# Optimization experiments

Measured on AMD Instinct MI355X. Metric: run time of the kernel, lower is better.

Reference implementation:

```python
import jax, jax.numpy as jnp
import numpy as np

B, D_IN, D_OUT, HID = 65536, 512, 512, 1024
LEVELS = (1, 4, 16)
BASE_LR = 0.1
LN_EPS = 1e-5


def setup_inputs() -> dict:
    key = jax.random.key(0)
    ks = jax.random.split(key, 20)
    s_in = 1.0 / np.sqrt(D_IN)
    s_h = 1.0 / np.sqrt(HID)
    inp = {
        'x': jax.random.normal(ks[0], (B, D_IN), dtype=jnp.float32),
        'global_step': 16,
        # CMS: 3 residual MLPs (d_in -> hid -> d_in)
        'cms_w1': jax.random.normal(ks[1], (3, HID, D_IN), dtype=jnp.float32) * s_in,
        'cms_b1': jnp.zeros((3, HID), dtype=jnp.float32),
        'cms_w2': jax.random.normal(ks[2], (3, D_IN, HID), dtype=jnp.float32) * s_h,
        'cms_b2': jnp.zeros((3, D_IN), dtype=jnp.float32),
        # gate generator
        'g_metab_w': jax.random.normal(ks[3], (HID, D_IN), dtype=jnp.float32) * s_in,
        'g_metab_b': jnp.zeros((HID,), dtype=jnp.float32),
        'g_sens_w': jax.random.normal(ks[4], (HID, D_IN), dtype=jnp.float32) * s_in,
        'g_sens_b': jnp.zeros((HID,), dtype=jnp.float32),
        'g_gate_w': jax.random.normal(ks[5], (HID, D_IN), dtype=jnp.float32) * s_in,
        'g_gate_b': jnp.zeros((HID,), dtype=jnp.float32),
        'g_out_w': jax.random.normal(ks[6], (3, HID), dtype=jnp.float32) * s_h,
        'g_out_b': jnp.zeros((3,), dtype=jnp.float32),
        # slow / fast weights, layernorm
        'W_slow': jax.random.normal(ks[7], (D_OUT, D_IN), dtype=jnp.float32) * (1.4 * s_in),
        'W_fast': jax.random.normal(ks[8], (D_OUT, D_IN), dtype=jnp.float32) * 0.01,
        'ln_gamma': jnp.ones((D_OUT,), dtype=jnp.float32),
        'ln_beta': jnp.zeros((D_OUT,), dtype=jnp.float32),
    }
    return inp


def reference(x, global_step, cms_w1, cms_b1, cms_w2, cms_b2,
              g_metab_w, g_metab_b, g_sens_w, g_sens_b, g_gate_w, g_gate_b,
              g_out_w, g_out_b, W_slow, W_fast, ln_gamma, ln_beta):
    # --- ContinuumMemorySystem: frequency-gated residual MLPs ---
    out = x
    for i, freq in enumerate(LEVELS):
        if global_step % freq == 0:
            h = jax.nn.relu(jnp.einsum('bd,hd->bh', out, cms_w1[i]) + cms_b1[i])
            out = jnp.einsum('bh,dh->bd', h, cms_w2[i]) + cms_b2[i] + out
    x_cms = out  # [B, D_IN]

    # --- SelfModifyingGates ---
    metab_h = jax.nn.sigmoid(jnp.einsum('bd,hd->bh', x_cms, g_metab_w) + g_metab_b)
    sens_h = jax.nn.sigmoid(jnp.einsum('bd,hd->bh', x_cms, g_sens_w) + g_sens_b)
    gate_h = jax.nn.sigmoid(jnp.einsum('bd,hd->bh', x_cms, g_gate_w) + g_gate_b)
    gates = jax.nn.sigmoid(jnp.einsum('bh,oh->bo', metab_h + sens_h + gate_h, g_out_w) + g_out_b)  # [B,3]
    metab, sens, gate = gates[:, 0], gates[:, 1], gates[:, 2]

    # --- slow / fast paths ---
    slow = jnp.einsum('bd,od->bo', x_cms, W_slow)   # [B, D_OUT]
    fast = jnp.einsum('bd,od->bo', x_cms, W_fast)   # [B, D_OUT]

    # --- Hebbian fast-weight update (no_grad in original) ---
    hebb = jnp.einsum('bo,bd->od', fast, x_cms) / x_cms.shape[0]     # [D_OUT, D_IN]
    forget = jnp.mean(fast ** 2, axis=0)[:, None] * W_fast           # [D_OUT, D_IN]
    rate = jnp.mean(metab) * BASE_LR
    new_W_fast = W_fast + jnp.tanh(hebb - forget) * rate

    # --- combine, per-sample-beta swish, layernorm ---
    combined = slow + fast * gate[:, None]
    beta = 0.5 + sens[:, None] * 2.0
    act = combined * jax.nn.sigmoid(beta * combined)
    mu = jnp.mean(act, axis=-1, keepdims=True)
    var = jnp.mean((act - mu) ** 2, axis=-1, keepdims=True)
    ln_out = (act - mu) * jax.lax.rsqrt(var + LN_EPS) * ln_gamma + ln_beta

    stats = jnp.stack([jnp.mean(metab), jnp.mean(sens), jnp.mean(gate)])
    return ln_out, new_W_fast, stats
```

## Files before the change

### kernel.cpp

```cpp
#include <hip/hip_runtime.h>
#include <hip/hip_bf16.h>
#include <cstdint>
#include <cstddef>

#define NB 65536
#define DD 512
#define HH 1024

typedef __attribute__((ext_vector_type(8))) short short8;
typedef __attribute__((ext_vector_type(4))) short short4v;
typedef __attribute__((ext_vector_type(4))) float f32x4;

__device__ __forceinline__ float bf2f(short s){
  union { float f; unsigned u; } v; v.u = ((unsigned)(unsigned short)s) << 16; return v.f;
}
__device__ __forceinline__ short f2bf(float f){
  union { float f; unsigned u; } v; v.f = f;
  unsigned u = v.u;
  u += 0x7FFFu + ((u >> 16) & 1u);
  return (short)(u >> 16);
}
__device__ __forceinline__ float sigm(float x){ return 1.0f / (1.0f + __expf(-x)); }

__device__ __forceinline__ float rowsum16(float v){
  int x;
  x = __builtin_amdgcn_update_dpp(0, __float_as_int(v), 0x128, 0xF, 0xF, true); v += __int_as_float(x);
  x = __builtin_amdgcn_update_dpp(0, __float_as_int(v), 0x124, 0xF, 0xF, true); v += __int_as_float(x);
  x = __builtin_amdgcn_update_dpp(0, __float_as_int(v), 0x122, 0xF, 0xF, true); v += __int_as_float(x);
  x = __builtin_amdgcn_update_dpp(0, __float_as_int(v), 0x121, 0xF, 0xF, true); v += __int_as_float(x);
  return v;
}

__device__ __forceinline__ int2 xcd_remap(int NX, int G){
  int flat = blockIdx.y*NX + blockIdx.x;
  int l = (flat & 7)*(G>>3) + (flat>>3);
  return make_int2(l / NX, l % NX);
}

#define GLL(srcp, dstp) \
  __builtin_amdgcn_global_load_lds((const __attribute__((address_space(1))) void*)(srcp), \
                                   (__attribute__((address_space(3))) void*)(dstp), 16, 0, 0)

__device__ __forceinline__ void stage128x32s(const short* __restrict__ g, int row0, int ldk, int k0,
                                             short* lds_base, int wave, int lane){
  const int pl = lane>>3, Gp = lane&7;
  const int Gl = Gp ^ pl;
  const int rconst = pl + ((Gl>>2)<<6);
  const int kg = (Gl&3)*8;
#pragma unroll
  for (int i = 0; i < 2; ++i){
    int c = wave*2 + i;
    const short* src = g + (size_t)(row0 + c*8 + rconst)*(size_t)ldk + (size_t)(k0 + kg);
    GLL(src, lds_base + c*512);
  }
}

template<int KTOT>
__device__ __forceinline__ void gemm128(const short* __restrict__ A, const short* __restrict__ W,
        int m0, int n0, short* smem, f32x4 acc[4][4], int wave, int lane)
{
  const int lr = lane & 15, lq = lane>>4;
  const int hiA = wave>>1, hiB = wave&1;
  int aOff[4], bOff[4];
#pragma unroll
  for (int i=0;i<4;++i){
    int pa = i*16 + lr;
    aOff[i] =        pa*64 + (((hiA*4+lq) ^ (pa&7))<<3);
    bOff[i] = 4096 + pa*64 + (((hiB*4+lq) ^ (pa&7))<<3);
  }
  stage128x32s(A, m0, KTOT, 0, smem,        wave, lane);
  stage128x32s(W, n0, KTOT, 0, smem + 4096, wave, lane);
  asm volatile("s_waitcnt vmcnt(0)" ::: "memory");
  __builtin_amdgcn_s_barrier();
  int cur = 0;
#pragma unroll
  for (int k0 = 0; k0 < KTOT; k0 += 32){
    short* buf  = smem + cur*8192;
    short* nbuf = smem + (cur^1)*8192;
    if (k0 + 32 < KTOT){
      stage128x32s(A, m0, KTOT, k0+32, nbuf,        wave, lane);
      stage128x32s(W, n0, KTOT, k0+32, nbuf + 4096, wave, lane);
    }
    short8 af[4], bf[4];
#pragma unroll
    for (int i=0;i<4;++i) af[i] = *(const short8*)&buf[aOff[i]];
#pragma unroll
    for (int i=0;i<4;++i) bf[i] = *(const short8*)&buf[bOff[i]];
    __builtin_amdgcn_s_setprio(1);
#pragma unroll
    for (int mi=0;mi<4;++mi)
#pragma unroll
      for (int ni=0;ni<4;++ni)
        acc[mi][ni] = __builtin_amdgcn_mfma_f32_16x16x32_bf16(af[mi], bf[ni], acc[mi][ni], 0, 0, 0);
    __builtin_amdgcn_s_setprio(0);
    asm volatile("s_waitcnt vmcnt(0)" ::: "memory");
    __builtin_amdgcn_s_barrier();
    cur ^= 1;
  }
}

#define ZERO_ACC(acc) \
  _Pragma("unroll") for (int zi=0;zi<4;++zi) _Pragma("unroll") for (int zj=0;zj<4;++zj) \
    acc[zi][zj] = (f32x4){0.f,0.f,0.f,0.f};

__global__ __launch_bounds__(256, 4) void k_gemm_h(const int* __restrict__ gs, int freq,
     const short* __restrict__ A, const short* __restrict__ W1, const float* __restrict__ b1,
     short* __restrict__ Hout)
{
  if (gs[0] % freq) return;
  __shared__ __align__(16) short smem[16384];
  const int tid = threadIdx.x, wave = tid>>6, lane = tid&63;
  int2 r = xcd_remap(8, 4096);
  const int m0 = r.x*128, n0 = r.y*128;
  f32x4 acc[4][4]; ZERO_ACC(acc);
  gemm128<DD>(A, W1, m0, n0, smem, acc, wave, lane);
  const int wm=(wave>>1)*64, wn=(wave&1)*64;
  const int rbase = m0 + wm + ((lane>>4)<<2);
  const int cbase = n0 + wn + (lane&15);
#pragma unroll
  for (int ni=0;ni<4;++ni){
    const float bias = b1[cbase + ni*16];
#pragma unroll
    for (int mi=0;mi<4;++mi)
#pragma unroll
      for (int rr=0;rr<4;++rr){
        float v = acc[mi][ni][rr] + bias;
        v = v > 0.f ? v : 0.f;
        Hout[(size_t)(rbase + mi*16 + rr)*HH + (cbase + ni*16)] = f2bf(v);
      }
  }
}

__global__ __launch_bounds__(256, 4) void k_gemm_res(const int* __restrict__ gs, int freq,
     const short* __restrict__ Hb, const short* __restrict__ W2, const float* __restrict__ b2,
     short* __restrict__ outb)
{
  if (gs[0] % freq) return;
  __shared__ __align__(16) short smem[16384];
  const int tid = threadIdx.x, wave = tid>>6, lane = tid&63;
  int2 r = xcd_remap(4, 2048);
  const int m0 = r.x*128, n0 = r.y*128;
  f32x4 acc[4][4]; ZERO_ACC(acc);
  gemm128<HH>(Hb, W2, m0, n0, smem, acc, wave, lane);
  const int wm=(wave>>1)*64, wn=(wave&1)*64;
  const int rbase = m0 + wm + ((lane>>4)<<2);
  const int cbase = n0 + wn + (lane&15);
#pragma unroll
  for (int ni=0;ni<4;++ni){
    const float bias = b2[cbase + ni*16];
#pragma unroll
    for (int mi=0;mi<4;++mi)
#pragma unroll
      for (int rr=0;rr<4;++rr){
        size_t off = (size_t)(rbase + mi*16 + rr)*DD + (cbase + ni*16);
        float v = acc[mi][ni][rr] + bias + bf2f(outb[off]);
        outb[off] = f2bf(v);
      }
  }
}

__global__ __launch_bounds__(256, 4) void k_gates(const short* __restrict__ A, const short* __restrict__ WG,
     const float* __restrict__ bm, const float* __restrict__ bs, const float* __restrict__ bg,
     const float* __restrict__ gow, float* __restrict__ pacc)
{
  __shared__ __align__(16) short smem[16384];
  __shared__ float sred[2][128][3];
  const int tid = threadIdx.x, wave = tid>>6, lane = tid&63;
  const int wmh = wave>>1, wnh = wave&1, lr = lane&15, lq = lane>>4;
  int2 r = xcd_remap(24, 12288);
  const int m0 = r.x*128, xj = r.y;
  const int j = xj >> 3, nb = xj & 7;
  const int n0 = nb*128;
  f32x4 acc[4][4]; ZERO_ACC(acc);
  gemm128<DD>(A, WG + (size_t)j*HH*DD, m0, n0, smem, acc, wave, lane);
  const int cb = n0 + wnh*64 + lr;
  const float* bj = (j==0) ? bm : ((j==1) ? bs : bg);
  float gw0[4], gw1[4], gw2[4], bias[4];
#pragma unroll
  for (int nf=0;nf<4;++nf){
    gw0[nf]  = gow[cb + nf*16];
    gw1[nf]  = gow[1024 + cb + nf*16];
    gw2[nf]  = gow[2048 + cb + nf*16];
    bias[nf] = bj[cb + nf*16];
  }
#pragma unroll
  for (int mf=0;mf<4;++mf)
#pragma unroll
    for (int rr=0;rr<4;++rr){
      float s0=0.f, s1=0.f, s2=0.f;
#pragma unroll
      for (int nf=0;nf<4;++nf){
        float v = sigm(acc[mf][nf][rr] + bias[nf]);
        s0 += v*gw0[nf]; s1 += v*gw1[nf]; s2 += v*gw2[nf];
      }
      s0 = rowsum16(s0); s1 = rowsum16(s1); s2 = rowsum16(s2);
      if (lr == 0){
        int lrow = wmh*64 + mf*16 + lq*4 + rr;
        sred[wnh][lrow][0] = s0;
        sred[wnh][lrow][1] = s1;
        sred[wnh][lrow][2] = s2;
      }
    }
  __syncthreads();
  if (tid < 128){
    float* dst = &pacc[((size_t)xj*NB + m0 + tid)*3];
    dst[0] = sred[0][tid][0] + sred[1][tid][0];
    dst[1] = sred[0][tid][1] + sred[1][tid][1];
    dst[2] = sred[0][tid][2] + sred[1][tid][2];
  }
}

__global__ __launch_bounds__(256, 4) void k_slowfast(const short* __restrict__ A,
     const short* __restrict__ WSF,
     short* __restrict__ SB, short* __restrict__ FB, float* __restrict__ f2sum)
{
  __shared__ __align__(16) short smem[16384];
  __shared__ float f2red[128];
  const int tid = threadIdx.x, wave = tid>>6, lane = tid&63;
  int2 r = xcd_remap(8, 4096);
  const int m0 = r.x*128, n0 = r.y*128;
  const bool isfast = (n0 >= 512);
  if (isfast){
    if (tid < 128) f2red[tid] = 0.f;
  }
  f32x4 acc[4][4]; ZERO_ACC(acc);
  gemm128<DD>(A, WSF, m0, n0, smem, acc, wave, lane);
  const int wm=(wave>>1)*64, wn=(wave&1)*64;
  const int rbase = m0 + wm + ((lane>>4)<<2);
  const int ccol0 = wn + (lane&15);
  if (!isfast){
#pragma unroll
    for (int ni=0;ni<4;++ni)
#pragma unroll
      for (int mi=0;mi<4;++mi)
#pragma unroll
        for (int rr=0;rr<4;++rr)
          SB[(size_t)(rbase + mi*16 + rr)*DD + (n0 + ccol0 + ni*16)] = f2bf(acc[mi][ni][rr]);
  } else {
#pragma unroll
    for (int ni=0;ni<4;++ni){
      float p = 0.f;
      const int fcol = n0 + ccol0 + ni*16 - 512;
#pragma unroll
      for (int mi=0;mi<4;++mi)
#pragma unroll
        for (int rr=0;rr<4;++rr){
          float fv = acc[mi][ni][rr];
          FB[(size_t)(rbase + mi*16 + rr)*DD + fcol] = f2bf(fv);
          p += fv*fv;
        }
      atomicAdd(&f2red[ccol0 + ni*16], p);
    }
    __syncthreads();
    if (tid < 128) atomicAdd(&f2sum[(n0-512) + tid], f2red[tid]);
  }
}

__global__ __launch_bounds__(256) void k_hebb(const short* __restrict__ FB,
     const short* __restrict__ XB, float* __restrict__ hebb)
{
  __shared__ __align__(16) short sT[10240];
  const int tid = threadIdx.x, wave = tid>>6, lane = tid&63;
  const int o0 = blockIdx.x*128, d0 = blockIdx.y*128;
  const int bz = blockIdx.z;
  const int tr = tid>>3;
  const int tc = (tid&7)*16;
  const int wm=(wave>>1)*64, wn=(wave&1)*64;
  const int lr = lane & 15, lk = (lane>>4)*8;
  f32x4 acc[4][4];
#pragma unroll
  for (int zi=0;zi<4;++zi)
#pragma unroll
    for (int zj=0;zj<4;++zj) acc[zi][zj] = (f32x4){0.f,0.f,0.f,0.f};
  for (int bb=0; bb<2048; bb+=32){
    const int b0 = bz*2048 + bb;
    __syncthreads();
#pragma unroll
    for (int h=0; h<2; ++h){
      short8 v = *(const short8*)&FB[(size_t)(b0+tr)*DD + o0 + tc + h*8];
#pragma unroll
      for (int j=0;j<8;++j) sT[(tc+h*8+j)*40 + tr] = v[j];
      short8 u = *(const short8*)&XB[(size_t)(b0+tr)*DD + d0 + tc + h*8];
#pragma unroll
      for (int j=0;j<8;++j) sT[5120 + (tc+h*8+j)*40 + tr] = u[j];
    }
    __syncthreads();
    short8 af[4], bf[4];
#pragma unroll
    for (int i=0;i<4;++i) af[i] = *(const short8*)&sT[(wm + i*16 + lr)*40 + lk];
#pragma unroll
    for (int i=0;i<4;++i) bf[i] = *(const short8*)&sT[5120 + (wn + i*16 + lr)*40 + lk];
#pragma unroll
    for (int mi=0;mi<4;++mi)
#pragma unroll
      for (int ni=0;ni<4;++ni)
        acc[mi][ni] = __builtin_amdgcn_mfma_f32_16x16x32_bf16(af[mi], bf[ni], acc[mi][ni], 0,0,0);
  }
  const int rbase = o0 + wm + ((lane>>4)<<2);
  const int cbase = d0 + wn + (lane&15);
#pragma unroll
  for (int mi=0;mi<4;++mi)
#pragma unroll
    for (int ni=0;ni<4;++ni)
#pragma unroll
      for (int r=0;r<4;++r)
        atomicAdd(&hebb[(size_t)(rbase + mi*16 + r)*DD + (cbase + ni*16)], acc[mi][ni][r]);
}

__global__ __launch_bounds__(256) void k_gatefin(const float* __restrict__ pacc,
     const float* __restrict__ gob,
     float* __restrict__ sensb, float* __restrict__ gateb, float* __restrict__ sacc)
{
  __shared__ float red[3][256];
  const int tid = threadIdx.x;
  const int row = blockIdx.x*256 + tid;
  float a0=0.f, a1=0.f, a2=0.f;
#pragma unroll
  for (int sidx=0; sidx<24; ++sidx){
    const float* p = &pacc[((size_t)sidx*NB + row)*3];
    a0 += p[0]; a1 += p[1]; a2 += p[2];
  }
  float m = sigm(a0 + gob[0]);
  float s = sigm(a1 + gob[1]);
  float g = sigm(a2 + gob[2]);
  sensb[row] = s; gateb[row] = g;
  red[0][tid]=m; red[1][tid]=s; red[2][tid]=g;
  __syncthreads();
  for (int off=128; off; off>>=1){
    if (tid < off){
      red[0][tid]+=red[0][tid+off];
      red[1][tid]+=red[1][tid+off];
      red[2][tid]+=red[2][tid+off];
    }
    __syncthreads();
  }
  if (tid < 3) atomicAdd(&sacc[tid], red[tid][0]);
}

__global__ __launch_bounds__(256) void k_epilogue(const short* __restrict__ SB, const short* __restrict__ FB,
     const float* __restrict__ gate, const float* __restrict__ sens,
     const float* __restrict__ gam, const float* __restrict__ bet, float* __restrict__ out,
     const float* __restrict__ hebb, const float* __restrict__ f2sum, const float* __restrict__ sacc,
     const float* __restrict__ Wf, float* __restrict__ outw, float* __restrict__ outstats)
{
  const int tid = threadIdx.x;
  if (blockIdx.x >= 16384){
    const int idx = (blockIdx.x - 16384)*256 + tid;
    const float inv = 1.f/65536.f;
    const float rate = sacc[0] * inv * 0.1f;
    const int o = idx >> 9;
    float w = Wf[idx];
    float h = hebb[idx] * inv;
    float forget = f2sum[o] * inv * w;
    outw[idx] = w + tanhf(h - forget) * rate;
    if (idx < 3) outstats[idx] = sacc[idx] * inv;
    return;
  }
  const int wave = tid>>6, lane = tid&63;
  const int row = blockIdx.x*4 + wave;
  const float g = gate[row], s = sens[row];
  const float bcoef = 0.5f + 2.0f*s;
  const int c0 = lane*8;
  short8 sv = *(const short8*)&SB[(size_t)row*DD + c0];
  short8 fv = *(const short8*)&FB[(size_t)row*DD + c0];
  float a[8]; float sum = 0.f;
#pragma unroll
  for (int j=0;j<8;++j){
    float c = bf2f(sv[j]) + bf2f(fv[j])*g;
    float av = c * sigm(bcoef*c);
    a[j] = av; sum += av;
  }
  for (int off=32; off; off>>=1) sum += __shfl_down(sum, off);
  sum = __shfl(sum, 0);
  const float mu = sum * (1.f/512.f);
  float vs = 0.f;
#pragma unroll
  for (int j=0;j<8;++j){ float d=a[j]-mu; vs += d*d; }
  for (int off=32; off; off>>=1) vs += __shfl_down(vs, off);
  vs = __shfl(vs, 0);
  const float rstd = rsqrtf(vs*(1.f/512.f) + 1e-5f);
  f32x4 o0, o1;
#pragma unroll
  for (int j=0;j<4;++j) o0[j] = (a[j]-mu)*rstd*gam[c0+j] + bet[c0+j];
#pragma unroll
  for (int j=0;j<4;++j) o1[j] = (a[4+j]-mu)*rstd*gam[c0+4+j] + bet[c0+4+j];
  *(f32x4*)&out[(size_t)row*DD + c0]     = o0;
  *(f32x4*)&out[(size_t)row*DD + c0 + 4] = o1;
}

__global__ __launch_bounds__(256) void k_castall(
     const float* __restrict__ w1, const float* __restrict__ w2,
     const float* __restrict__ gmw, const float* __restrict__ gsw, const float* __restrict__ ggw,
     const float* __restrict__ wslow, const float* __restrict__ wfast,
     short* __restrict__ wcW1, short* __restrict__ wcW2, short* __restrict__ wcG,
     short* __restrict__ wcWSF,
     const float* __restrict__ x, short* __restrict__ outb)
{
  const int b = blockIdx.x, t = threadIdx.x;
  if (b >= 20480){
    const int i = (b - 20480)*256 + t;
    f32x4 v = *(const f32x4*)&x[(size_t)i*4];
    short4v bb;
#pragma unroll
    for (int j=0;j<4;++j) bb[j] = f2bf(v[j]);
    *(short4v*)&outb[(size_t)i*4] = bb;
    return;
  }
  const float* src; short* dst; int off;
  if      (b < 6144)  { src=w1;    dst=wcW1;           off=b; }
  else if (b < 12288) { src=w2;    dst=wcW2;           off=b-6144; }
  else if (b < 14336) { src=gmw;   dst=wcG;            off=b-12288; }
  else if (b < 16384) { src=gsw;   dst=wcG+524288;     off=b-14336; }
  else if (b < 18432) { src=ggw;   dst=wcG+1048576;    off=b-16384; }
  else if (b < 19456) { src=wslow; dst=wcWSF;          off=b-18432; }
  else                { src=wfast; dst=wcWSF+262144;   off=b-19456; }
  const int i = off*256 + t;
  dst[i] = f2bf(src[i]);
}

extern "C" void kernel_launch(void* const* d_in, const int* in_sizes, int n_in,
                              void* d_out, int out_size, void* d_ws, size_t ws_size,
                              hipStream_t stream)
{
  const float* x    = (const float*)d_in[0];
  const int*   gs   = (const int*)d_in[1];
  const float* w1   = (const float*)d_in[2];
  const float* b1   = (const float*)d_in[3];
  const float* w2   = (const float*)d_in[4];
  const float* b2   = (const float*)d_in[5];
  const float* gmw  = (const float*)d_in[6];
  const float* gmb  = (const float*)d_in[7];
  const float* gsw  = (const float*)d_in[8];
  const float* gsb  = (const float*)d_in[9];
  const float* ggw  = (const float*)d_in[10];
  const float* ggb  = (const float*)d_in[11];
  const float* gow  = (const float*)d_in[12];
  const float* gob  = (const float*)d_in[13];
  const float* wslow= (const float*)d_in[14];
  const float* wfast= (const float*)d_in[15];
  const float* gam  = (const float*)d_in[16];
  const float* bet  = (const float*)d_in[17];

  char* ws = (char*)d_ws;
  short* outb  = (short*)(ws + 134217728);
  short* hbuf  = (short*)(ws + 201326592);
  short* wcW1  = (short*)(ws + 335544320);
  short* wcW2  = (short*)(ws + 338690048);
  short* wcG   = (short*)(ws + 341835776);
  short* wcWSF = (short*)(ws + 344981504);
  float* hebb  = (float*)(ws + 346030080);
  float* f2sum = (float*)(ws + 347078656);
  float* sacc  = (float*)(ws + 347080704);
  float* sensb = (float*)(ws + 347080960);
  float* gateb = (float*)(ws + 347343104);
  float* pacc  = (float*)(ws + 201326592);
  short* slowb = (short*)(ws + 0);
  short* fastb = (short*)(ws + 67108864);

  float* o_ln = (float*)d_out;
  float* o_wf = o_ln + (size_t)NB*DD;
  float* o_st = o_wf + 262144;

  hipMemsetAsync(hebb, 0, 1048576, stream);
  hipMemsetAsync(f2sum, 0, 2048, stream);
  hipMemsetAsync(sacc, 0, 256, stream);

  k_castall<<<dim3(53248),256,0,stream>>>(w1, w2, gmw, gsw, ggw, wslow, wfast,
                                          wcW1, wcW2, wcG, wcWSF, x, outb);

  const int freqs[3] = {1,4,16};
  for (int lv=0; lv<3; ++lv){
    k_gemm_h  <<<dim3(8,512),256,0,stream>>>(gs, freqs[lv], outb, wcW1 + (size_t)lv*524288, b1 + lv*HH, hbuf);
    k_gemm_res<<<dim3(4,512),256,0,stream>>>(gs, freqs[lv], hbuf, wcW2 + (size_t)lv*524288, b2 + lv*DD, outb);
  }

  k_gates   <<<dim3(24,512),256,0,stream>>>(outb, wcG, gmb, gsb, ggb, gow, pacc);
  k_gatefin <<<dim3(256),256,0,stream>>>(pacc, gob, sensb, gateb, sacc);
  k_slowfast<<<dim3(8,512),256,0,stream>>>(outb, wcWSF, slowb, fastb, f2sum);
  k_hebb    <<<dim3(4,4,32),256,0,stream>>>(fastb, outb, hebb);
  k_epilogue<<<dim3(17408),256,0,stream>>>(slowb, fastb, gateb, sensb, gam, bet, o_ln,
                                           hebb, f2sum, sacc, wfast, o_wf, o_st);
}
```

Before: 1.288 ms.

## Quantize gate GEMM inputs to int8 and use i8 MFMA

Adds per-row int8 quantization kernels for the CMS output and the three gate weight matrices, then rewrites the gate GEMM to use mfma_i32_16x16x64_i8 with double-buffered LDS staging and dequantization in the epilogue. The aim is to halve operand bytes and use the higher int8 MFMA throughput for the largest GEMM. This adds an extra quantization pass over the activations and loses precision in the gate values, which feed the outputs.

```diff
diff --git a/kernel.cpp b/kernel.cpp
--- a/kernel.cpp
+++ b/kernel.cpp
@@ -10,6 +10,7 @@
 typedef __attribute__((ext_vector_type(8))) short short8;
 typedef __attribute__((ext_vector_type(4))) short short4v;
 typedef __attribute__((ext_vector_type(4))) float f32x4;
+typedef __attribute__((ext_vector_type(4))) int int4v;
 
 __device__ __forceinline__ float bf2f(short s){
   union { float f; unsigned u; } v; v.u = ((unsigned)(unsigned short)s) << 16; return v.f;
@@ -52,6 +53,20 @@
     int c = wave*2 + i;
     const short* src = g + (size_t)(row0 + c*8 + rconst)*(size_t)ldk + (size_t)(k0 + kg);
     GLL(src, lds_base + c*512);
+  }
+}
+
+__device__ __forceinline__ void stage128x64q(const char* __restrict__ g, int k0B,
+                                             char* lds_base, int wave, int lane){
+  const int pl = lane>>3, Gp = lane&7;
+  const int Gl = Gp ^ pl;
+  const int rconst = pl + ((Gl>>2)<<6);
+  const int kg = (Gl&3)*16;
+#pragma unroll
+  for (int i = 0; i < 2; ++i){
+    int c = wave*2 + i;
+    const char* src = g + (size_t)(c*8 + rconst)*512 + (size_t)(k0B + kg);
+    GLL(src, lds_base + c*1024);
   }
 }
 
@@ -159,38 +174,136 @@
   }
 }
 
-__global__ __launch_bounds__(256, 4) void k_gates(const short* __restrict__ A, const short* __restrict__ WG,
+__global__ __launch_bounds__(256) void k_quantx(const short* __restrict__ outb,
+     char* __restrict__ x8, float* __restrict__ sxr)
+{
+  const int tid = threadIdx.x, wave = tid>>6, lane = tid&63;
+  const int row = blockIdx.x*4 + wave;
+  short8 v = *(const short8*)&outb[(size_t)row*DD + lane*8];
+  float f[8]; float m = 0.f;
+#pragma unroll
+  for (int j=0;j<8;++j){ f[j] = bf2f(v[j]); m = fmaxf(m, fabsf(f[j])); }
+#pragma unroll
+  for (int off=32; off; off>>=1) m = fmaxf(m, __shfl_xor(m, off));
+  m = fmaxf(m, 1e-20f);
+  const float inv = 127.0f / m;
+  unsigned lo=0, hi=0;
+#pragma unroll
+  for (int j=0;j<4;++j){ int q=(int)rintf(f[j]*inv); q=q>127?127:(q<-127?-127:q); lo |= ((unsigned)(q&255))<<(8*j); }
+#pragma unroll
+  for (int j=0;j<4;++j){ int q=(int)rintf(f[4+j]*inv); q=q>127?127:(q<-127?-127:q); hi |= ((unsigned)(q&255))<<(8*j); }
+  int2 w; w.x=(int)lo; w.y=(int)hi;
+  *(int2*)&x8[(size_t)row*DD + lane*8] = w;
+  if (lane==0) sxr[row] = m * (1.0f/127.0f);
+}
+
+__global__ __launch_bounds__(256) void k_quantw(const float* __restrict__ gmw,
+     const float* __restrict__ gsw, const float* __restrict__ ggw,
+     char* __restrict__ W8, float* __restrict__ swr)
+{
+  const int tid = threadIdx.x, wave = tid>>6, lane = tid&63;
+  const int row = blockIdx.x*4 + wave;
+  const int j = row >> 10;
+  const float* src = (j==0?gmw:(j==1?gsw:ggw)) + (size_t)(row&1023)*DD + lane*8;
+  f32x4 a = *(const f32x4*)&src[0];
+  f32x4 b = *(const f32x4*)&src[4];
+  float f[8] = {a[0],a[1],a[2],a[3],b[0],b[1],b[2],b[3]};
+  float m = 0.f;
+#pragma unroll
+  for (int k=0;k<8;++k) m = fmaxf(m, fabsf(f[k]));
+#pragma unroll
+  for (int off=32; off; off>>=1) m = fmaxf(m, __shfl_xor(m, off));
+  m = fmaxf(m, 1e-20f);
+  const float inv = 127.0f / m;
+  unsigned lo=0, hi=0;
+#pragma unroll
+  for (int k=0;k<4;++k){ int q=(int)rintf(f[k]*inv); q=q>127?127:(q<-127?-127:q); lo |= ((unsigned)(q&255))<<(8*k); }
+#pragma unroll
+  for (int k=0;k<4;++k){ int q=(int)rintf(f[4+k]*inv); q=q>127?127:(q<-127?-127:q); hi |= ((unsigned)(q&255))<<(8*k); }
+  int2 w; w.x=(int)lo; w.y=(int)hi;
+  *(int2*)&W8[(size_t)row*DD + lane*8] = w;
+  if (lane==0) swr[row] = m * (1.0f/127.0f);
+}
+
+__global__ __launch_bounds__(256, 4) void k_gates(const char* __restrict__ X8, const char* __restrict__ W8,
+     const float* __restrict__ sxr, const float* __restrict__ swr,
      const float* __restrict__ bm, const float* __restrict__ bs, const float* __restrict__ bg,
      const float* __restrict__ gow, float* __restrict__ pacc)
 {
-  __shared__ __align__(16) short smem[16384];
+  __shared__ __align__(16) char smemc[32768];
   __shared__ float sred[2][128][3];
   const int tid = threadIdx.x, wave = tid>>6, lane = tid&63;
   const int wmh = wave>>1, wnh = wave&1, lr = lane&15, lq = lane>>4;
   int2 r = xcd_remap(24, 12288);
   const int m0 = r.x*128, xj = r.y;
-  const int j = xj >> 3, nb = xj & 7;
-  const int n0 = nb*128;
-  f32x4 acc[4][4]; ZERO_ACC(acc);
-  gemm128<DD>(A, WG + (size_t)j*HH*DD, m0, n0, smem, acc, wave, lane);
+  const int j = xj >> 3;
+  const int n0 = (xj & 7)*128;
+  int aOff[4], bOff[4];
+#pragma unroll
+  for (int i=0;i<4;++i){
+    int pa = i*16 + lr;
+    aOff[i] =        pa*128 + (((wmh*4+lq) ^ (pa&7))<<4);
+    bOff[i] = 8192 + pa*128 + (((wnh*4+lq) ^ (pa&7))<<4);
+  }
+  const char* aS = X8 + (size_t)m0*DD;
+  const char* bS = W8 + (size_t)xj*128*DD;
+  int4v acc[4][4];
+#pragma unroll
+  for (int zi=0;zi<4;++zi)
+#pragma unroll
+    for (int zj=0;zj<4;++zj) acc[zi][zj] = (int4v){0,0,0,0};
+
+  stage128x64q(aS, 0, smemc,        wave, lane);
+  stage128x64q(bS, 0, smemc + 8192, wave, lane);
+  asm volatile("s_waitcnt vmcnt(0)" ::: "memory");
+  __builtin_amdgcn_s_barrier();
+  int cur = 0;
+#pragma unroll
+  for (int kt = 0; kt < 8; ++kt){
+    char* buf  = smemc + cur*16384;
+    char* nbuf = smemc + (cur^1)*16384;
+    if (kt + 1 < 8){
+      stage128x64q(aS, (kt+1)*64, nbuf,        wave, lane);
+      stage128x64q(bS, (kt+1)*64, nbuf + 8192, wave, lane);
+    }
+    int4v af[4], bf[4];
+#pragma unroll
+    for (int i=0;i<4;++i) af[i] = *(const int4v*)&buf[aOff[i]];
+#pragma unroll
+    for (int i=0;i<4;++i) bf[i] = *(const int4v*)&buf[bOff[i]];
+    __builtin_amdgcn_s_setprio(1);
+#pragma unroll
+    for (int mi=0;mi<4;++mi)
+#pragma unroll
+      for (int ni=0;ni<4;++ni)
+        acc[mi][ni] = __builtin_amdgcn_mfma_i32_16x16x64_i8(af[mi], bf[ni], acc[mi][ni], 0, 0, 0);
+    __builtin_amdgcn_s_setprio(0);
+    asm volatile("s_waitcnt vmcnt(0)" ::: "memory");
+    __builtin_amdgcn_s_barrier();
+    cur ^= 1;
+  }
+
   const int cb = n0 + wnh*64 + lr;
+  const int rbase = m0 + wmh*64 + lq*4;
   const float* bj = (j==0) ? bm : ((j==1) ? bs : bg);
-  float gw0[4], gw1[4], gw2[4], bias[4];
+  float gw0[4], gw1[4], gw2[4], bias[4], sw[4];
 #pragma unroll
   for (int nf=0;nf<4;++nf){
     gw0[nf]  = gow[cb + nf*16];
     gw1[nf]  = gow[1024 + cb + nf*16];
     gw2[nf]  = gow[2048 + cb + nf*16];
     bias[nf] = bj[cb + nf*16];
+    sw[nf]   = swr[(size_t)xj*128 + wnh*64 + lr + nf*16];
   }
 #pragma unroll
   for (int mf=0;mf<4;++mf)
 #pragma unroll
     for (int rr=0;rr<4;++rr){
+      const float sx = sxr[rbase + mf*16 + rr];
       float s0=0.f, s1=0.f, s2=0.f;
 #pragma unroll
       for (int nf=0;nf<4;++nf){
-        float v = sigm(acc[mf][nf][rr] + bias[nf]);
+        float v = sigm((float)acc[mf][nf][rr] * (sx * sw[nf]) + bias[nf]);
         s0 += v*gw0[nf]; s1 += v*gw1[nf]; s2 += v*gw2[nf];
       }
       s0 = rowsum16(s0); s1 = rowsum16(s1); s2 = rowsum16(s2);
@@ -390,15 +503,13 @@
 
 __global__ __launch_bounds__(256) void k_castall(
      const float* __restrict__ w1, const float* __restrict__ w2,
-     const float* __restrict__ gmw, const float* __restrict__ gsw, const float* __restrict__ ggw,
      const float* __restrict__ wslow, const float* __restrict__ wfast,
-     short* __restrict__ wcW1, short* __restrict__ wcW2, short* __restrict__ wcG,
-     short* __restrict__ wcWSF,
+     short* __restrict__ wcW1, short* __restrict__ wcW2, short* __restrict__ wcWSF,
      const float* __restrict__ x, short* __restrict__ outb)
 {
   const int b = blockIdx.x, t = threadIdx.x;
-  if (b >= 20480){
-    const int i = (b - 20480)*256 + t;
+  if (b >= 14336){
+    const int i = (b - 14336)*256 + t;
     f32x4 v = *(const f32x4*)&x[(size_t)i*4];
     short4v bb;
 #pragma unroll
@@ -409,11 +520,8 @@
   const float* src; short* dst; int off;
   if      (b < 6144)  { src=w1;    dst=wcW1;           off=b; }
   else if (b < 12288) { src=w2;    dst=wcW2;           off=b-6144; }
-  else if (b < 14336) { src=gmw;   dst=wcG;            off=b-12288; }
-  else if (b < 16384) { src=gsw;   dst=wcG+524288;     off=b-14336; }
-  else if (b < 18432) { src=ggw;   dst=wcG+1048576;    off=b-16384; }
-  else if (b < 19456) { src=wslow; dst=wcWSF;          off=b-18432; }
-  else                { src=wfast; dst=wcWSF+262144;   off=b-19456; }
+  else if (b < 13312) { src=wslow; dst=wcWSF;          off=b-12288; }
+  else                { src=wfast; dst=wcWSF+262144;   off=b-13312; }
   const int i = off*256 + t;
   dst[i] = f2bf(src[i]);
 }
@@ -442,17 +550,20 @@
   const float* bet  = (const float*)d_in[17];
 
   char* ws = (char*)d_ws;
+  char*  x8    = (char*)(ws + 0);
   short* outb  = (short*)(ws + 134217728);
   short* hbuf  = (short*)(ws + 201326592);
   short* wcW1  = (short*)(ws + 335544320);
   short* wcW2  = (short*)(ws + 338690048);
-  short* wcG   = (short*)(ws + 341835776);
+  char*  W8    = (char*)(ws + 341835776);
   short* wcWSF = (short*)(ws + 344981504);
   float* hebb  = (float*)(ws + 346030080);
   float* f2sum = (float*)(ws + 347078656);
   float* sacc  = (float*)(ws + 347080704);
   float* sensb = (float*)(ws + 347080960);
   float* gateb = (float*)(ws + 347343104);
+  float* sxr   = (float*)(ws + 347605248);
+  float* swr   = (float*)(ws + 347867392);
   float* pacc  = (float*)(ws + 201326592);
   short* slowb = (short*)(ws + 0);
   short* fastb = (short*)(ws + 67108864);
@@ -465,8 +576,9 @@
   hipMemsetAsync(f2sum, 0, 2048, stream);
   hipMemsetAsync(sacc, 0, 256, stream);
 
-  k_castall<<<dim3(53248),256,0,stream>>>(w1, w2, gmw, gsw, ggw, wslow, wfast,
-                                          wcW1, wcW2, wcG, wcWSF, x, outb);
+  k_castall<<<dim3(47104),256,0,stream>>>(w1, w2, wslow, wfast,
+                                          wcW1, wcW2, wcWSF, x, outb);
+  k_quantw<<<dim3(768),256,0,stream>>>(gmw, gsw, ggw, W8, swr);
 
   const int freqs[3] = {1,4,16};
   for (int lv=0; lv<3; ++lv){
@@ -474,10 +586,11 @@
     k_gemm_res<<<dim3(4,512),256,0,stream>>>(gs, freqs[lv], hbuf, wcW2 + (size_t)lv*524288, b2 + lv*DD, outb);
   }
 
-  k_gates   <<<dim3(24,512),256,0,stream>>>(outb, wcG, gmb, gsb, ggb, gow, pacc);
-  k_gatefin <<<dim3(256),256,0,stream>>>(pacc, gob, sensb, gateb, sacc);
+  k_quantx <<<dim3(16384),256,0,stream>>>(outb, x8, sxr);
+  k_gates  <<<dim3(24,512),256,0,stream>>>(x8, W8, sxr, swr, gmb, gsb, ggb, gow, pacc);
+  k_gatefin<<<dim3(256),256,0,stream>>>(pacc, gob, sensb, gateb, sacc);
   k_slowfast<<<dim3(8,512),256,0,stream>>>(outb, wcWSF, slowb, fastb, f2sum);
-  k_hebb    <<<dim3(4,4,32),256,0,stream>>>(fastb, outb, hebb);
+  k_hebb   <<<dim3(4,4,32),256,0,stream>>>(fastb, outb, hebb);
   k_epilogue<<<dim3(17408),256,0,stream>>>(slowb, fastb, gateb, sensb, gam, bet, o_ln,
                                            hebb, f2sum, sacc, wfast, o_wf, o_st);
 }
```

New measurement: 1.220 ms (median of 2 runs). 5.3% less time.
